# Kernel optimization log

Measured on AMD Instinct MI355X. Metric: run time of the kernel, lower is better.

Reference implementation:

```python
import jax, jax.numpy as jnp
import numpy as np

N_VARS = 100
MAX_LAG = 10
HIDDEN = 64
E = N_VARS * MAX_LAG  # number of tiny expert MLPs
BATCH = 4096


def setup_inputs() -> dict:
    key = jax.random.key(0)
    k_x, k_w1, k_b1, k_w2, k_b2 = jax.random.split(key, 5)
    x = jax.random.normal(k_x, (BATCH, E), dtype=jnp.float32)
    # PyTorch Linear(1, H): weight [H,1] -> stacked as [E, H]; bias [E, H]
    lim1 = 1.0  # kaiming-uniform-ish bound for fan_in=1
    W1 = jax.random.uniform(k_w1, (E, HIDDEN), dtype=jnp.float32, minval=-lim1, maxval=lim1)
    b1 = jax.random.uniform(k_b1, (E, HIDDEN), dtype=jnp.float32, minval=-lim1, maxval=lim1)
    # Linear(H, n_vars): weight [n_vars,H] -> stacked as [E, H, n_vars]; bias [E, n_vars]
    lim2 = 1.0 / np.sqrt(HIDDEN)
    W2 = jax.random.uniform(k_w2, (E, HIDDEN, N_VARS), dtype=jnp.float32, minval=-lim2, maxval=lim2)
    b2 = jax.random.uniform(k_b2, (E, N_VARS), dtype=jnp.float32, minval=-lim2, maxval=lim2)
    return {"x": x, "W1": W1, "b1": b1, "W2": W2, "b2": b2}


def reference(x, W1, b1, W2, b2):
    # Fused form of: sum_i Linear2_i(relu(Linear1_i(x[:, i:i+1])))
    # h[b,e,h] = relu(x[b,e] * W1[e,h] + b1[e,h])
    h = jax.nn.relu(x[:, :, None] * W1[None, :, :] + b1[None, :, :])  # [B,E,H]
    # sum over experts folded into the contraction: out[b,v] = sum_e h[b,e,:] @ W2[e,:,v]
    out = jnp.einsum("beh,ehv->bv", h, W2) + jnp.sum(b2, axis=0)  # [B,n_vars]
    return out
```

## Files before the change

### kernel.cpp

```cpp
#include <hip/hip_runtime.h>
#include <hip/hip_bf16.h>

#define NV 100
#define HID 64
#define NE 1000
#define NB 4096
#define ESPLIT 32
#define BLOBU 3712
#define EXPB 14848

typedef __attribute__((ext_vector_type(8))) short short8;
typedef __attribute__((ext_vector_type(4))) float f32x4;
typedef __attribute__((ext_vector_type(4))) unsigned short u16x4;

__device__ __align__(16) float g_bsum[NV];

__device__ __forceinline__ short cvtbf(float f) {
    return __builtin_bit_cast(short, (__bf16)f);
}
__device__ __forceinline__ unsigned short f2bf(float f) {
    return (unsigned short)__builtin_bit_cast(short, (__bf16)f);
}
__device__ __forceinline__ float bf2f(unsigned short s) {
    union { unsigned u; float f; } v; v.u = ((unsigned)s) << 16;
    return v.f;
}
__device__ __forceinline__ unsigned pkbf(float a, float b) {
    return (unsigned)f2bf(a) | ((unsigned)f2bf(b) << 16);
}

__device__ __host__ __forceinline__ void esplit_range(int ks, int* pe0, int* pne) {
    int e0 = (ks < 26) ? 32 * ks : 832 + 28 * (ks - 26);
    int ne = (ks < 26) ? 32 : 28;
    *pe0 = e0; *pne = ne;
}

__global__ void bias_kernel(const float* __restrict__ b2) {
    int v = blockIdx.x;
    float s = 0.f;
    for (int e = threadIdx.x; e < NE; e += 256)
        s += b2[e * NV + v];
    __shared__ float red[4];
    for (int off = 32; off; off >>= 1) s += __shfl_down(s, off, 64);
    if ((threadIdx.x & 63) == 0) red[threadIdx.x >> 6] = s;
    __syncthreads();
    if (threadIdx.x == 0) g_bsum[v] = red[0] + red[1] + red[2] + red[3];
}

__global__ void init_kernel(float* __restrict__ out) {
    int idx = blockIdx.x * 256 + threadIdx.x;
    if (idx < NB * NV) out[idx] = g_bsum[idx % NV];
}

__global__ void prepass6(const float* __restrict__ W2, const float* __restrict__ W1,
                         const float* __restrict__ b1, unsigned* __restrict__ blob) {
    __shared__ float t[HID][NV + 1];
    int e = blockIdx.x;
    const float* src = W2 + (size_t)e * (HID * NV);
    for (int i = threadIdx.x; i < HID * NV; i += 256) {
        int hh = i / NV;
        int v = i - hh * NV;
        t[hh][v] = src[i];
    }
    __syncthreads();
    unsigned* dst = blob + (size_t)e * BLOBU;
    for (int o = threadIdx.x; o < 3584; o += 256) {
        int f = o >> 8;
        int r = o & 255;
        int l = r >> 2;
        int q = r & 3;
        int ksh = f / 7, tt = f - 7 * ksh;
        int kg = l >> 4, lrow = l & 15;
        int h0 = ksh * 32 + kg * 8 + 2 * q;
        int v = tt * 16 + lrow;
        unsigned val = 0;
        if (v < NV) val = pkbf(t[h0][v], t[h0 + 1][v]);
        dst[o] = val;
    }
    if (threadIdx.x < 128) {
        int o = threadIdx.x;
        int ksh = o >> 6, kg = (o >> 4) & 3, j = o & 15;
        int h0 = ksh * 32 + kg * 8;
        float val = (j < 8) ? W1[(size_t)e * HID + h0 + j]
                            : b1[(size_t)e * HID + h0 + (j - 8)];
        dst[3584 + o] = __builtin_bit_cast(unsigned, val);
    }
}

__global__ __launch_bounds__(256, 2) void moe9(
    const float* __restrict__ x, const unsigned* __restrict__ blob,
    float* __restrict__ part)
{
    __shared__ __align__(16) unsigned char smem[4 * EXPB + 16384];
    unsigned short* xts = (unsigned short*)(smem + 4 * EXPB);

    const int bid = blockIdx.x;
    const int xcd = bid & 7;
    const int jj  = bid >> 3;
    const int ks  = xcd * 4 + (jj & 3);
    const int mb  = jj >> 2;

    const int tid  = threadIdx.x;
    const int lane = tid & 63;
    const int wave = tid >> 6;
    const int lrow = lane & 15;
    const int kg   = lane >> 4;

    const int row0 = mb * 256;
    int e0, ne; esplit_range(ks, &e0, &ne);

    {
        int r = tid;
        int slot = (r >> 6) * 64 + (r & 15) * 4 + ((r >> 4) & 3);
        const float* xp = x + (size_t)(row0 + r) * NE + e0;
        #pragma unroll
        for (int c4 = 0; c4 < 8; ++c4) {
            int eb = c4 * 4;
            if (eb < ne) {
                float4 v = *(const float4*)(xp + eb);
                xts[(eb + 0) * 256 + slot] = f2bf(v.x);
                xts[(eb + 1) * 256 + slot] = f2bf(v.y);
                xts[(eb + 2) * 256 + slot] = f2bf(v.z);
                xts[(eb + 3) * 256 + slot] = f2bf(v.w);
            }
        }
    }

    auto stage2 = [&](int buf, int e) {
        const unsigned* g = blob + (size_t)e * BLOBU;
        unsigned* lbase = (unsigned*)(smem + buf * (2 * EXPB));
        #pragma unroll
        for (int k = 0; k < 7; ++k) {
            int off = (k * 256 + tid) * 4;
            __builtin_amdgcn_global_load_lds(
                (const __attribute__((address_space(1))) unsigned*)(g + off),
                (__attribute__((address_space(3))) unsigned*)(lbase + off),
                16, 0, 0);
        }
        if (tid < 64) {
            int off = (1792 + tid) * 4;
            __builtin_amdgcn_global_load_lds(
                (const __attribute__((address_space(1))) unsigned*)(g + off),
                (__attribute__((address_space(3))) unsigned*)(lbase + off),
                16, 0, 0);
        }
    };

    stage2(0, e0);
    __syncthreads();

    f32x4 acc[4][7];
    #pragma unroll
    for (int rf = 0; rf < 4; ++rf)
        #pragma unroll
        for (int t = 0; t < 7; ++t)
            acc[rf][t] = (f32x4){0.f, 0.f, 0.f, 0.f};

    auto do_expert = [&](const unsigned char* ebase, int ei) {
        u16x4 xq = *(const u16x4*)&xts[ei * 256 + wave * 64 + lrow * 4];
        float xv[4];
        #pragma unroll
        for (int rf = 0; rf < 4; ++rf) xv[rf] = bf2f(xq[rf]);

        #pragma unroll
        for (int ksh = 0; ksh < 2; ++ksh) {
            const float4* wpk = (const float4*)(ebase + 14336 + (ksh * 4 + kg) * 64);
            float4 wa = wpk[0];
            float4 wb = wpk[1];
            float4 ba = wpk[2];
            float4 bb = wpk[3];

            short8 afr[4];
            #pragma unroll
            for (int rf = 0; rf < 4; ++rf) {
                float xr = xv[rf];
                short8 a;
                a[0] = cvtbf(fmaxf(fmaf(xr, wa.x, ba.x), 0.f));
                a[1] = cvtbf(fmaxf(fmaf(xr, wa.y, ba.y), 0.f));
                a[2] = cvtbf(fmaxf(fmaf(xr, wa.z, ba.z), 0.f));
                a[3] = cvtbf(fmaxf(fmaf(xr, wa.w, ba.w), 0.f));
                a[4] = cvtbf(fmaxf(fmaf(xr, wb.x, bb.x), 0.f));
                a[5] = cvtbf(fmaxf(fmaf(xr, wb.y, bb.y), 0.f));
                a[6] = cvtbf(fmaxf(fmaf(xr, wb.z, bb.z), 0.f));
                a[7] = cvtbf(fmaxf(fmaf(xr, wb.w, bb.w), 0.f));
                afr[rf] = a;
            }

            __builtin_amdgcn_s_setprio(1);
            #pragma unroll
            for (int t = 0; t < 7; ++t) {
                short8 bf = *(const short8*)(ebase + ((ksh * 7 + t) << 10) + lane * 16);
                #pragma unroll
                for (int rf = 0; rf < 4; ++rf)
                    acc[rf][t] = __builtin_amdgcn_mfma_f32_16x16x32_bf16(afr[rf], bf, acc[rf][t], 0, 0, 0);
            }
            __builtin_amdgcn_s_setprio(0);
        }
    };

    int cur = 0;
    const int npairs = ne >> 1;
    for (int p = 0; p < npairs; ++p) {
        if (p + 1 < npairs) stage2(cur ^ 1, e0 + 2 * (p + 1));

        const unsigned char* bufc = smem + cur * (2 * EXPB);
        do_expert(bufc, 2 * p);
        do_expert(bufc + EXPB, 2 * p + 1);

        __syncthreads();
        cur ^= 1;
    }

    float* dst = part + (size_t)ks * (NB * NV);
    #pragma unroll
    for (int rf = 0; rf < 4; ++rf) {
        #pragma unroll
        for (int t = 0; t < 7; ++t) {
            int col = t * 16 + lrow;
            if (col < NV) {
                size_t base = (size_t)(row0 + wave * 64 + rf * 16 + kg * 4) * NV + col;
                #pragma unroll
                for (int r = 0; r < 4; ++r)
                    dst[base + (size_t)r * NV] = acc[rf][t][r];
            }
        }
    }
}

__global__ void reduce2(const float* __restrict__ part, float* __restrict__ out) {
    int i4 = blockIdx.x * 256 + threadIdx.x;
    f32x4 s = *(const f32x4*)&g_bsum[(i4 % 25) * 4];
    size_t off = (size_t)i4 * 4;
    #pragma unroll 4
    for (int k = 0; k < ESPLIT; ++k)
        s += *(const f32x4*)&part[(size_t)k * (NB * NV) + off];
    *(f32x4*)&out[off] = s;
}

#define LDW 72
__global__ __launch_bounds__(256, 3) void moe_fallback(
    const float* __restrict__ x, const float* __restrict__ W1,
    const float* __restrict__ b1, const float* __restrict__ W2,
    float* __restrict__ dst)
{
    __shared__ unsigned short w2t[8192];
    const int tid  = threadIdx.x;
    const int lane = tid & 63;
    const int lrow = lane & 15;
    const int kg   = lane >> 4;
    const int wave = tid >> 6;
    const int row0 = blockIdx.x * 128 + wave * 32;
    const int e0 = blockIdx.y * 32;
    const int e1 = min(NE, e0 + 32);

    f32x4 acc[2][7];
    #pragma unroll
    for (int rf = 0; rf < 2; ++rf)
        #pragma unroll
        for (int t = 0; t < 7; ++t)
            acc[rf][t] = (f32x4){0.f, 0.f, 0.f, 0.f};

    const float* xr0 = x + (size_t)(row0 + lrow) * NE;
    const float* xr1 = x + (size_t)(row0 + 16 + lrow) * NE;

    for (int e = e0; e < e1; ++e) {
        __syncthreads();
        const float* src = W2 + (size_t)e * (HID * NV);
        unsigned* w2t32 = (unsigned*)w2t;
        #pragma unroll
        for (int k = 0; k < 13; ++k) {
            int i = tid + k * 256;
            if (i < (HID / 2) * NV) {
                int a3  = i / 400;
                int rem = i - a3 * 400;
                int bv  = rem >> 2;
                int c   = rem & 3;
                int hh2 = a3 * 4 + c;
                float f0 = src[(2 * hh2) * NV + bv];
                float f1 = src[(2 * hh2 + 1) * NV + bv];
                w2t32[bv * (LDW / 2) + hh2] = pkbf(f0, f1);
            }
        }
        __syncthreads();

        float xv0 = xr0[e];
        float xv1 = xr1[e];
        const float* w1p = W1 + e * HID;
        const float* b1p = b1 + e * HID;
        #pragma unroll
        for (int ksh = 0; ksh < 2; ++ksh) {
            const int hb = ksh * 32 + kg * 8;
            f32x4 w1lo = *(const f32x4*)(w1p + hb);
            f32x4 w1hi = *(const f32x4*)(w1p + hb + 4);
            f32x4 blo  = *(const f32x4*)(b1p + hb);
            f32x4 bhi  = *(const f32x4*)(b1p + hb + 4);
            short8 a0, a1;
            #pragma unroll
            for (int j = 0; j < 4; ++j) {
                a0[j]     = cvtbf(fmaxf(fmaf(xv0, w1lo[j], blo[j]), 0.f));
                a0[j + 4] = cvtbf(fmaxf(fmaf(xv0, w1hi[j], bhi[j]), 0.f));
                a1[j]     = cvtbf(fmaxf(fmaf(xv1, w1lo[j], blo[j]), 0.f));
                a1[j + 4] = cvtbf(fmaxf(fmaf(xv1, w1hi[j], bhi[j]), 0.f));
            }
            #pragma unroll
            for (int t = 0; t < 7; ++t) {
                short8 bf = *(const short8*)&w2t[(t * 16 + lrow) * LDW + hb];
                acc[0][t] = __builtin_amdgcn_mfma_f32_16x16x32_bf16(a0, bf, acc[0][t], 0, 0, 0);
                acc[1][t] = __builtin_amdgcn_mfma_f32_16x16x32_bf16(a1, bf, acc[1][t], 0, 0, 0);
            }
        }
    }

    #pragma unroll
    for (int rf = 0; rf < 2; ++rf) {
        #pragma unroll
        for (int t = 0; t < 7; ++t) {
            int col = t * 16 + lrow;
            if (col < NV) {
                size_t base = (size_t)(row0 + rf * 16 + kg * 4) * NV + col;
                #pragma unroll
                for (int r = 0; r < 4; ++r)
                    atomicAdd(&dst[base + (size_t)r * NV], acc[rf][t][r]);
            }
        }
    }
}

extern "C" void kernel_launch(void* const* d_in, const int* in_sizes, int n_in,
                              void* d_out, int out_size, void* d_ws, size_t ws_size,
                              hipStream_t stream) {
    const float* x  = (const float*)d_in[0];
    const float* W1 = (const float*)d_in[1];
    const float* b1 = (const float*)d_in[2];
    const float* W2 = (const float*)d_in[3];
    const float* b2 = (const float*)d_in[4];
    float* out = (float*)d_out;

    const size_t BLOB_BYTES = (size_t)NE * BLOBU * 4;
    const size_t PART_BYTES = (size_t)ESPLIT * NB * NV * 4;

    bias_kernel<<<NV, 256, 0, stream>>>(b2);

    if (ws_size >= BLOB_BYTES + PART_BYTES) {
        unsigned* blob = (unsigned*)d_ws;
        float* part = (float*)((char*)d_ws + BLOB_BYTES);
        prepass6<<<NE, 256, 0, stream>>>(W2, W1, b1, blob);
        moe9<<<512, 256, 0, stream>>>(x, blob, part);
        reduce2<<<(NB * NV / 4 + 255) / 256, 256, 0, stream>>>(part, out);
    } else {
        init_kernel<<<(NB * NV + 255) / 256, 256, 0, stream>>>(out);
        moe_fallback<<<dim3(NB / 128, ESPLIT), 256, 0, stream>>>(x, W1, b1, W2, out);
    }
}
```

Before: 81.57 us.

## Load W1/b1 directly from global in main kernel and stagger block start

```diff
diff --git a/kernel.cpp b/kernel.cpp
--- a/kernel.cpp
+++ b/kernel.cpp
@@ -6,8 +6,8 @@
 #define NE 1000
 #define NB 4096
 #define ESPLIT 32
-#define BLOBU 3712
-#define EXPB 14848
+#define BLOBU 3584
+#define EXPB 14336
 
 typedef __attribute__((ext_vector_type(8))) short short8;
 typedef __attribute__((ext_vector_type(4))) float f32x4;
@@ -52,8 +52,7 @@
     if (idx < NB * NV) out[idx] = g_bsum[idx % NV];
 }
 
-__global__ void prepass6(const float* __restrict__ W2, const float* __restrict__ W1,
-                         const float* __restrict__ b1, unsigned* __restrict__ blob) {
+__global__ void prepass7(const float* __restrict__ W2, unsigned* __restrict__ blob) {
     __shared__ float t[HID][NV + 1];
     int e = blockIdx.x;
     const float* src = W2 + (size_t)e * (HID * NV);
@@ -64,7 +63,7 @@
     }
     __syncthreads();
     unsigned* dst = blob + (size_t)e * BLOBU;
-    for (int o = threadIdx.x; o < 3584; o += 256) {
+    for (int o = threadIdx.x; o < BLOBU; o += 256) {
         int f = o >> 8;
         int r = o & 255;
         int l = r >> 2;
@@ -77,18 +76,11 @@
         if (v < NV) val = pkbf(t[h0][v], t[h0 + 1][v]);
         dst[o] = val;
     }
-    if (threadIdx.x < 128) {
-        int o = threadIdx.x;
-        int ksh = o >> 6, kg = (o >> 4) & 3, j = o & 15;
-        int h0 = ksh * 32 + kg * 8;
-        float val = (j < 8) ? W1[(size_t)e * HID + h0 + j]
-                            : b1[(size_t)e * HID + h0 + (j - 8)];
-        dst[3584 + o] = __builtin_bit_cast(unsigned, val);
-    }
-}
-
-__global__ __launch_bounds__(256, 2) void moe9(
-    const float* __restrict__ x, const unsigned* __restrict__ blob,
+}
+
+__global__ __launch_bounds__(256, 2) void moe10(
+    const float* __restrict__ x, const float* __restrict__ W1,
+    const float* __restrict__ b1, const unsigned* __restrict__ blob,
     float* __restrict__ part)
 {
     __shared__ __align__(16) unsigned char smem[4 * EXPB + 16384];
@@ -137,17 +129,12 @@
                 (__attribute__((address_space(3))) unsigned*)(lbase + off),
                 16, 0, 0);
         }
-        if (tid < 64) {
-            int off = (1792 + tid) * 4;
-            __builtin_amdgcn_global_load_lds(
-                (const __attribute__((address_space(1))) unsigned*)(g + off),
-                (__attribute__((address_space(3))) unsigned*)(lbase + off),
-                16, 0, 0);
-        }
     };
 
     stage2(0, e0);
     __syncthreads();
+
+    if ((bid >> 8) & 1) __builtin_amdgcn_s_sleep(64);
 
     f32x4 acc[4][7];
     #pragma unroll
@@ -156,7 +143,7 @@
         for (int t = 0; t < 7; ++t)
             acc[rf][t] = (f32x4){0.f, 0.f, 0.f, 0.f};
 
-    auto do_expert = [&](const unsigned char* ebase, int ei) {
+    auto do_expert = [&](const unsigned char* ebase, int ei, const float4* Wf) {
         u16x4 xq = *(const u16x4*)&xts[ei * 256 + wave * 64 + lrow * 4];
         float xv[4];
         #pragma unroll
@@ -164,11 +151,10 @@
 
         #pragma unroll
         for (int ksh = 0; ksh < 2; ++ksh) {
-            const float4* wpk = (const float4*)(ebase + 14336 + (ksh * 4 + kg) * 64);
-            float4 wa = wpk[0];
-            float4 wb = wpk[1];
-            float4 ba = wpk[2];
-            float4 bb = wpk[3];
+            float4 wa = Wf[ksh * 4 + 0];
+            float4 wb = Wf[ksh * 4 + 1];
+            float4 ba = Wf[ksh * 4 + 2];
+            float4 bb = Wf[ksh * 4 + 3];
 
             short8 afr[4];
             #pragma unroll
@@ -203,9 +189,27 @@
     for (int p = 0; p < npairs; ++p) {
         if (p + 1 < npairs) stage2(cur ^ 1, e0 + 2 * (p + 1));
 
+        const int eA = e0 + 2 * p, eB = eA + 1;
+        float4 WA[8], WB[8];
+        #pragma unroll
+        for (int ksh = 0; ksh < 2; ++ksh) {
+            const float* w1p = W1 + (size_t)eA * HID + ksh * 32 + kg * 8;
+            const float* b1p = b1 + (size_t)eA * HID + ksh * 32 + kg * 8;
+            WA[ksh * 4 + 0] = *(const float4*)(w1p);
+            WA[ksh * 4 + 1] = *(const float4*)(w1p + 4);
+            WA[ksh * 4 + 2] = *(const float4*)(b1p);
+            WA[ksh * 4 + 3] = *(const float4*)(b1p + 4);
+            const float* w1q = W1 + (size_t)eB * HID + ksh * 32 + kg * 8;
+            const float* b1q = b1 + (size_t)eB * HID + ksh * 32 + kg * 8;
+            WB[ksh * 4 + 0] = *(const float4*)(w1q);
+            WB[ksh * 4 + 1] = *(const float4*)(w1q + 4);
+            WB[ksh * 4 + 2] = *(const float4*)(b1q);
+            WB[ksh * 4 + 3] = *(const float4*)(b1q + 4);
+        }
+
         const unsigned char* bufc = smem + cur * (2 * EXPB);
-        do_expert(bufc, 2 * p);
-        do_expert(bufc + EXPB, 2 * p + 1);
+        do_expert(bufc, 2 * p, WA);
+        do_expert(bufc + EXPB, 2 * p + 1, WB);
 
         __syncthreads();
         cur ^= 1;
@@ -344,8 +348,8 @@
     if (ws_size >= BLOB_BYTES + PART_BYTES) {
         unsigned* blob = (unsigned*)d_ws;
         float* part = (float*)((char*)d_ws + BLOB_BYTES);
-        prepass6<<<NE, 256, 0, stream>>>(W2, W1, b1, blob);
-        moe9<<<512, 256, 0, stream>>>(x, blob, part);
+        prepass7<<<NE, 256, 0, stream>>>(W2, blob);
+        moe10<<<512, 256, 0, stream>>>(x, W1, b1, blob, part);
         reduce2<<<(NB * NV / 4 + 255) / 256, 256, 0, stream>>>(part, out);
     } else {
         init_kernel<<<(NB * NV + 255) / 256, 256, 0, stream>>>(out);
```

After: 86.71 us. 6.3% more time.
